# Kernel optimization log

Hardware: AMD Instinct MI355X
Metric: run time of the kernel (lower is better)

The kernel has to match this reference:

```python
import jax, jax.numpy as jnp
import numpy as np


def _conv1x1(x, W, b):
    # 1x1 conv == per-pixel channel matmul: x [B,C,H,W], W [O,C], b [O]
    return jnp.einsum('bchw,oc->bohw', x, W) + b[None, :, None, None]


def setup_inputs() -> dict:
    key = jax.random.key(0)
    ks = jax.random.split(key, 9)
    B, C, H, W = 16, 512, 32, 32
    s = 1.0 / np.sqrt(C)
    inp = {
        'x': jax.random.normal(ks[0], (B, C, H, W), dtype=jnp.float32),
        'Wq': jax.random.normal(ks[1], (C, C), dtype=jnp.float32) * s,
        'bq': jax.random.normal(ks[2], (C,), dtype=jnp.float32) * 0.01,
        'Wk': jax.random.normal(ks[3], (C, C), dtype=jnp.float32) * s,
        'bk': jax.random.normal(ks[4], (C,), dtype=jnp.float32) * 0.01,
        'Wv': jax.random.normal(ks[5], (C, C), dtype=jnp.float32) * s,
        'bv': jax.random.normal(ks[6], (C,), dtype=jnp.float32) * 0.01,
        'Wo': jax.random.normal(ks[7], (C, C), dtype=jnp.float32) * s,
        'bo': jax.random.normal(ks[8], (C,), dtype=jnp.float32) * 0.01,
    }
    return inp


def reference(x, Wq, bq, Wk, bk, Wv, bv, Wo, bo):
    B, C, H, W = x.shape
    q = _conv1x1(x, Wq, bq)
    k = _conv1x1(x, Wk, bk)
    v = _conv1x1(x, Wv, bv)
    hw = H * W
    qf = q.reshape(B, C, hw)  # [B,C,HW]
    kf = k.reshape(B, C, hw)
    vf = v.reshape(B, C, hw)
    # scores[b,i,j] = sum_c q[b,c,i] * k[b,c,j], scaled by c^-0.5
    scores = jnp.einsum('bci,bcj->bij', qf, kf) * (C ** -0.5)
    attn = jax.nn.softmax(scores, axis=2)  # softmax over keys j
    # out[b,c,i] = sum_j v[b,c,j] * attn[b,i,j]
    out = jnp.einsum('bcj,bij->bci', vf, attn).reshape(B, C, H, W)
    out = _conv1x1(out, Wo, bo)
    return x + out
```

## Files before the change

kernel.cpp:

```cpp
#include <hip/hip_runtime.h>
#include <hip/hip_bf16.h>
#include <math.h>


typedef __bf16 bf16x8 __attribute__((ext_vector_type(8)));
typedef float  f32x16 __attribute__((ext_vector_type(16)));

__device__ __forceinline__ unsigned short f2bf(float f) {
    unsigned u = __float_as_uint(f);
    u += 0x7fff + ((u >> 16) & 1);
    return (unsigned short)(u >> 16);
}

__device__ __forceinline__ void gload_lds16(const void* g, void* l) {
    __builtin_amdgcn_global_load_lds(
        (const __attribute__((address_space(1))) void*)g,
        (__attribute__((address_space(3))) void*)l, 16, 0, 0);
}

struct GemmP {
    const unsigned short* A;
    const unsigned short* B;
    void* C;
    const float* bias;
    const float* resid;
    int M, N, K, ldA, ldB;
    long sA, sB, sC, sR;
    int ln_nn, ln_pb;
    float scale;
};

template<bool OUT_F32, int BIAS_MODE, bool RESID, int EXPM>
__device__ __forceinline__ void gemm_body(const GemmP p, int L,
                                          unsigned short* Als,
                                          unsigned short* Bls)
{
    const int xcd = L & 7;
    const int idx = L >> 3;
    const int bz  = xcd * 2 + (idx >> p.ln_pb);
    const int w   = idx & ((1 << p.ln_pb) - 1);
    const int m0  = (w >> p.ln_nn) << 7;
    const int n0  = (w & ((1 << p.ln_nn) - 1)) << 8;

    const unsigned short* A = p.A + bz * p.sA;
    const unsigned short* B = p.B + bz * p.sB;

    const int tid  = threadIdx.x;
    const int lane = tid & 63;
    const int wave = tid >> 6;

    const int ar = lane >> 2;
    const int ak = (((lane & 3) ^ ((ar >> 1) & 3))) * 8;

    const unsigned short* agp = A + (long)(m0 + wave * 16 + ar) * p.ldA + ak;
    const unsigned short* bgp = B + (long)(n0 + wave * 16 + ar) * p.ldB + ak;
    const long aj = 64L * p.ldA;
    const long bj = 64L * p.ldB;

    const int ln31 = lane & 31;
    const int hi   = lane >> 5;
    const int swz  = ((ln31 >> 1) & 3) << 3;
    const int koff0 = (hi * 8) ^ swz;
    const int koff1 = (16 + hi * 8) ^ swz;

    f32x16 acc[4][2] = {};
    f32x16 acc1[4] = {};
    bf16x8 ones;
    if constexpr (EXPM == 2) {
        #pragma unroll
        for (int i = 0; i < 8; ++i) ones[i] = (__bf16)1.0f;
    }

    const int nsteps = p.K >> 5;

    auto STAGE = [&](int sel) {
        unsigned short* a0 = Als + sel * 4096;
        unsigned short* b0 = Bls + sel * 8192;
        gload_lds16(agp,          a0 + wave * 512);
        gload_lds16(agp + aj,     a0 + (wave + 4) * 512);
        gload_lds16(bgp,          b0 + wave * 512);
        gload_lds16(bgp + bj,     b0 + (wave + 4) * 512);
        gload_lds16(bgp + 2 * bj, b0 + (wave + 8) * 512);
        gload_lds16(bgp + 3 * bj, b0 + (wave + 12) * 512);
        agp += 32; bgp += 32;
    };

    auto COMPUTE = [&](int sel) {
        const unsigned short* Ap = Als + sel * 4096;
        const unsigned short* Bp = Bls + sel * 8192;
        #pragma unroll
        for (int ks = 0; ks < 2; ++ks) {
            const int ko = ks ? koff1 : koff0;
            bf16x8 af[4], bfr[2];
            #pragma unroll
            for (int mt = 0; mt < 4; ++mt)
                af[mt] = *(const bf16x8*)&Ap[(mt * 32 + ln31) * 32 + ko];
            #pragma unroll
            for (int nt = 0; nt < 2; ++nt)
                bfr[nt] = *(const bf16x8*)&Bp[(wave * 64 + nt * 32 + ln31) * 32 + ko];
            if constexpr (EXPM == 2) {
                #pragma unroll
                for (int mt = 0; mt < 4; ++mt)
                    acc1[mt] = __builtin_amdgcn_mfma_f32_32x32x16_bf16(
                        af[mt], ones, acc1[mt], 0, 0, 0);
            }
            #pragma unroll
            for (int mt = 0; mt < 4; ++mt)
                #pragma unroll
                for (int nt = 0; nt < 2; ++nt)
                    acc[mt][nt] = __builtin_amdgcn_mfma_f32_32x32x16_bf16(
                        af[mt], bfr[nt], acc[mt][nt], 0, 0, 0);
        }
    };

    STAGE(0);
    STAGE(1);

    int bc = 0, bn = 1, bs = 2;
    for (int t = 0; t < nsteps - 1; ++t) {
        __builtin_amdgcn_sched_barrier(0);
        asm volatile("s_waitcnt vmcnt(6)" ::: "memory");
        __builtin_amdgcn_s_barrier();
        asm volatile("" ::: "memory");
        __builtin_amdgcn_sched_barrier(0);
        if (t + 2 < nsteps) STAGE(bs);
        COMPUTE(bc);
        const int tmp = bc; bc = bn; bn = bs; bs = tmp;
    }
    __builtin_amdgcn_sched_barrier(0);
    asm volatile("s_waitcnt vmcnt(0)" ::: "memory");
    __builtin_amdgcn_s_barrier();
    asm volatile("" ::: "memory");
    __builtin_amdgcn_sched_barrier(0);
    COMPUTE(bc);

    float* Cf = (float*)p.C + bz * p.sC;
    unsigned short* Ch = (unsigned short*)p.C + bz * p.sC;
    const float* resid = RESID ? (p.resid + bz * p.sR) : nullptr;
    const int N = p.N;

    #pragma unroll
    for (int mt = 0; mt < 4; ++mt) {
        #pragma unroll
        for (int r = 0; r < 16; ++r) {
            const int row = m0 + mt * 32 + (r & 3) + 8 * (r >> 2) + 4 * hi;
            float rv = 0.0f;
            if constexpr (EXPM == 2) rv = 1.0f / acc1[mt][r];
            const float bm = (BIAS_MODE == 1) ? p.bias[row] : 0.0f;
            #pragma unroll
            for (int nt = 0; nt < 2; ++nt) {
                const int col = n0 + wave * 64 + nt * 32 + ln31;
                float val = acc[mt][nt][r];
                if constexpr (EXPM == 1) {
                    val = __expf(val * p.scale);
                } else {
                    if (BIAS_MODE == 1) val += bm;
                    if (BIAS_MODE == 2) val += p.bias[col];
                    if constexpr (EXPM == 2) val *= rv;
                }
                const long o = (long)row * N + col;
                if (RESID) val += resid[o];
                if (OUT_F32) Cf[o] = val;
                else         Ch[o] = f2bf(val);
            }
        }
    }
}

template<bool OUT_F32, int BIAS_MODE, bool RESID, int EXPM>
__global__ __launch_bounds__(256, 2) void gemm_bt_mfma(GemmP p)
{
    __shared__ unsigned short Als[3 * 4096];
    __shared__ unsigned short Bls[3 * 8192];
    gemm_body<OUT_F32, BIAS_MODE, RESID, EXPM>(p, blockIdx.x, Als, Bls);
}

__global__ __launch_bounds__(256, 2) void gemm_qkv_fused(GemmP pqk, GemmP pv, int split)
{
    __shared__ unsigned short Als[3 * 4096];
    __shared__ unsigned short Bls[3 * 8192];
    if ((int)blockIdx.x < split)
        gemm_body<false, 2, false, 0>(pqk, blockIdx.x, Als, Bls);
    else
        gemm_body<false, 1, false, 0>(pv, blockIdx.x - split, Als, Bls);
}

__global__ __launch_bounds__(256) void prep_all(
    const float* __restrict__ x, unsigned short* __restrict__ xT,
    const float* __restrict__ Wq, const float* __restrict__ Wk,
    const float* __restrict__ Wv, const float* __restrict__ Wo,
    const float* __restrict__ bq, const float* __restrict__ bk,
    unsigned short* __restrict__ Wb, float* __restrict__ biasqk)
{
    const int b = blockIdx.x;
    const int t = threadIdx.x;
    if (b < 8192) {
        __shared__ float tl[32][33];
        const int batch = b >> 9;
        const int rem = b & 511;
        const int p0 = (rem & 31) * 32;
        const int c0 = (rem >> 5) * 32;
        const float* xb = x + (long)batch * 524288;
        unsigned short* xTb = xT + (long)batch * 524288;
        const int tx = t & 31;
        const int ty = t >> 5;
        #pragma unroll
        for (int i = 0; i < 4; ++i)
            tl[ty + 8 * i][tx] = xb[(long)(c0 + ty + 8 * i) * 1024 + p0 + tx];
        __syncthreads();
        #pragma unroll
        for (int i = 0; i < 4; ++i)
            xTb[(long)(p0 + ty + 8 * i) * 512 + c0 + tx] = f2bf(tl[tx][ty + 8 * i]);
    } else if (b < 9216) {
        const int wb = b - 8192;
        const float* srcs[4] = {Wq, Wk, Wv, Wo};
        const float* s = srcs[wb >> 8];
        unsigned short* d = Wb + (long)(wb >> 8) * 262144;
        const int i = ((wb & 255) * 256 + t) * 4;
        const float4 f = *(const float4*)(s + i);
        ushort4 h;
        h.x = f2bf(f.x); h.y = f2bf(f.y); h.z = f2bf(f.z); h.w = f2bf(f.w);
        *(ushort4*)(d + i) = h;
    } else {
        biasqk[t]       = bq[t];
        biasqk[256 + t] = bq[256 + t];
        biasqk[512 + t] = bk[t];
        biasqk[768 + t] = bk[256 + t];
    }
}

extern "C" void kernel_launch(void* const* d_in, const int* in_sizes, int n_in,
                              void* d_out, int out_size, void* d_ws, size_t ws_size,
                              hipStream_t stream)
{
    const float* x  = (const float*)d_in[0];
    const float* Wq = (const float*)d_in[1];
    const float* bq = (const float*)d_in[2];
    const float* Wk = (const float*)d_in[3];
    const float* bk = (const float*)d_in[4];
    const float* Wv = (const float*)d_in[5];
    const float* bv = (const float*)d_in[6];
    const float* Wo = (const float*)d_in[7];
    const float* bo = (const float*)d_in[8];
    float* out = (float*)d_out;

    const int Bn = 16, C = 512, HW = 1024;
    const long CHW = (long)C * HW;
    const long SHW = (long)HW * HW;

    unsigned short* xT   = (unsigned short*)d_ws;
    unsigned short* qkT  = xT + Bn * CHW;
    unsigned short* vB   = qkT + Bn * SHW;
    unsigned short* expS = vB + Bn * CHW;
    unsigned short* Wb   = expS + Bn * SHW;
    float* biasqk = (float*)(Wb + 4 * 262144);
    unsigned short* OT = xT;

    unsigned short* Wvb = Wb + 2 * 262144;
    unsigned short* Wob = Wb + 3 * 262144;

    const dim3 blk(256);
    const float scale = 0.044194173824159216f;

    prep_all<<<dim3(9217), blk, 0, stream>>>(x, xT, Wq, Wk, Wv, Wo, bq, bk,
                                             Wb, biasqk);

    GemmP pqk = { xT, Wb, qkT, biasqk, nullptr,
                  HW, 2 * C, C, C, C, CHW, 0, SHW, 0, 2, 5, 0.0f };
    GemmP pv  = { Wvb, xT, vB, bv, nullptr,
                  C, HW, C, C, C, 0, CHW, CHW, 0, 2, 4, 0.0f };
    gemm_qkv_fused<<<dim3(768), blk, 0, stream>>>(pqk, pv, 512);

    GemmP ps  = { qkT, qkT + C, expS, nullptr, nullptr,
                  HW, HW, C, 2 * C, 2 * C, SHW, SHW, SHW, 0, 2, 5, scale };
    gemm_bt_mfma<false, 0, false, 1><<<dim3(512), blk, 0, stream>>>(ps);

    GemmP po  = { expS, vB, OT, nullptr, nullptr,
                  HW, C, HW, HW, HW, SHW, CHW, CHW, 0, 1, 4, 0.0f };
    gemm_bt_mfma<false, 0, false, 2><<<dim3(256), blk, 0, stream>>>(po);

    GemmP pout = { Wob, OT, out, bo, x,
                   C, HW, C, C, C, 0, CHW, CHW, CHW, 2, 4, 0.0f };
    gemm_bt_mfma<true, 1, true, 0><<<dim3(256), blk, 0, stream>>>(pout);
}
```

Baseline: 249.8 us.

## Switch GEMMs to 128x128 tiles with 16x16x32 MFMA and 2x2 wave grid

Shrinks the block output tile from 128x256 to 128x128, arranges the four waves as a 2x2 grid, and moves from 32x32x16 to 16x16x32 MFMA instructions. The LDS footprint per block is halved, launch bounds go from 2 to 3 blocks per CU, and every launch uses twice as many blocks, all aimed at better occupancy and load balance across CUs. It also drops the XOR swizzle on the LDS layout, which may bring back bank conflicts, and each block now reuses its A tile across a narrower N range. The epilogue is rewritten to match the new accumulator layout.

```diff
diff --git a/kernel.cpp b/kernel.cpp
--- a/kernel.cpp
+++ b/kernel.cpp
@@ -4,7 +4,7 @@
 
 
 typedef __bf16 bf16x8 __attribute__((ext_vector_type(8)));
-typedef float  f32x16 __attribute__((ext_vector_type(16)));
+typedef float  f32x4  __attribute__((ext_vector_type(4)));
 
 __device__ __forceinline__ unsigned short f2bf(float f) {
     unsigned u = __float_as_uint(f);
@@ -40,7 +40,7 @@
     const int bz  = xcd * 2 + (idx >> p.ln_pb);
     const int w   = idx & ((1 << p.ln_pb) - 1);
     const int m0  = (w >> p.ln_nn) << 7;
-    const int n0  = (w & ((1 << p.ln_nn) - 1)) << 8;
+    const int n0  = (w & ((1 << p.ln_nn) - 1)) << 7;
 
     const unsigned short* A = p.A + bz * p.sA;
     const unsigned short* B = p.B + bz * p.sB;
@@ -48,23 +48,22 @@
     const int tid  = threadIdx.x;
     const int lane = tid & 63;
     const int wave = tid >> 6;
+    const int wm   = wave >> 1;
+    const int wn   = wave & 1;
 
     const int ar = lane >> 2;
-    const int ak = (((lane & 3) ^ ((ar >> 1) & 3))) * 8;
+    const int ak = (lane & 3) * 8;
 
     const unsigned short* agp = A + (long)(m0 + wave * 16 + ar) * p.ldA + ak;
     const unsigned short* bgp = B + (long)(n0 + wave * 16 + ar) * p.ldB + ak;
     const long aj = 64L * p.ldA;
     const long bj = 64L * p.ldB;
 
-    const int ln31 = lane & 31;
-    const int hi   = lane >> 5;
-    const int swz  = ((ln31 >> 1) & 3) << 3;
-    const int koff0 = (hi * 8) ^ swz;
-    const int koff1 = (16 + hi * 8) ^ swz;
-
-    f32x16 acc[4][2] = {};
-    f32x16 acc1[4] = {};
+    const int fr = lane & 15;
+    const int fq = lane >> 4;
+
+    f32x4 acc[4][4] = {};
+    f32x4 acc1[4] = {};
     bf16x8 ones;
     if constexpr (EXPM == 2) {
         #pragma unroll
@@ -75,42 +74,36 @@
 
     auto STAGE = [&](int sel) {
         unsigned short* a0 = Als + sel * 4096;
-        unsigned short* b0 = Bls + sel * 8192;
-        gload_lds16(agp,          a0 + wave * 512);
-        gload_lds16(agp + aj,     a0 + (wave + 4) * 512);
-        gload_lds16(bgp,          b0 + wave * 512);
-        gload_lds16(bgp + bj,     b0 + (wave + 4) * 512);
-        gload_lds16(bgp + 2 * bj, b0 + (wave + 8) * 512);
-        gload_lds16(bgp + 3 * bj, b0 + (wave + 12) * 512);
+        unsigned short* b0 = Bls + sel * 4096;
+        gload_lds16(agp,      a0 + wave * 512);
+        gload_lds16(agp + aj, a0 + (wave + 4) * 512);
+        gload_lds16(bgp,      b0 + wave * 512);
+        gload_lds16(bgp + bj, b0 + (wave + 4) * 512);
         agp += 32; bgp += 32;
     };
 
     auto COMPUTE = [&](int sel) {
         const unsigned short* Ap = Als + sel * 4096;
-        const unsigned short* Bp = Bls + sel * 8192;
-        #pragma unroll
-        for (int ks = 0; ks < 2; ++ks) {
-            const int ko = ks ? koff1 : koff0;
-            bf16x8 af[4], bfr[2];
+        const unsigned short* Bp = Bls + sel * 4096;
+        bf16x8 af[4], bfr[4];
+        #pragma unroll
+        for (int mt = 0; mt < 4; ++mt)
+            af[mt] = *(const bf16x8*)&Ap[(wm * 64 + mt * 16 + fr) * 32 + fq * 8];
+        #pragma unroll
+        for (int nt = 0; nt < 4; ++nt)
+            bfr[nt] = *(const bf16x8*)&Bp[(wn * 64 + nt * 16 + fr) * 32 + fq * 8];
+        if constexpr (EXPM == 2) {
             #pragma unroll
             for (int mt = 0; mt < 4; ++mt)
-                af[mt] = *(const bf16x8*)&Ap[(mt * 32 + ln31) * 32 + ko];
-            #pragma unroll
-            for (int nt = 0; nt < 2; ++nt)
-                bfr[nt] = *(const bf16x8*)&Bp[(wave * 64 + nt * 32 + ln31) * 32 + ko];
-            if constexpr (EXPM == 2) {
-                #pragma unroll
-                for (int mt = 0; mt < 4; ++mt)
-                    acc1[mt] = __builtin_amdgcn_mfma_f32_32x32x16_bf16(
-                        af[mt], ones, acc1[mt], 0, 0, 0);
-            }
-            #pragma unroll
-            for (int mt = 0; mt < 4; ++mt)
-                #pragma unroll
-                for (int nt = 0; nt < 2; ++nt)
-                    acc[mt][nt] = __builtin_amdgcn_mfma_f32_32x32x16_bf16(
-                        af[mt], bfr[nt], acc[mt][nt], 0, 0, 0);
+                acc1[mt] = __builtin_amdgcn_mfma_f32_16x16x32_bf16(
+                    af[mt], ones, acc1[mt], 0, 0, 0);
         }
+        #pragma unroll
+        for (int mt = 0; mt < 4; ++mt)
+            #pragma unroll
+            for (int nt = 0; nt < 4; ++nt)
+                acc[mt][nt] = __builtin_amdgcn_mfma_f32_16x16x32_bf16(
+                    af[mt], bfr[nt], acc[mt][nt], 0, 0, 0);
     };
 
     STAGE(0);
@@ -119,7 +112,7 @@
     int bc = 0, bn = 1, bs = 2;
     for (int t = 0; t < nsteps - 1; ++t) {
         __builtin_amdgcn_sched_barrier(0);
-        asm volatile("s_waitcnt vmcnt(6)" ::: "memory");
+        asm volatile("s_waitcnt vmcnt(4)" ::: "memory");
         __builtin_amdgcn_s_barrier();
         asm volatile("" ::: "memory");
         __builtin_amdgcn_sched_barrier(0);
@@ -139,46 +132,59 @@
     const float* resid = RESID ? (p.resid + bz * p.sR) : nullptr;
     const int N = p.N;
 
-    #pragma unroll
-    for (int mt = 0; mt < 4; ++mt) {
-        #pragma unroll
-        for (int r = 0; r < 16; ++r) {
-            const int row = m0 + mt * 32 + (r & 3) + 8 * (r >> 2) + 4 * hi;
-            float rv = 0.0f;
-            if constexpr (EXPM == 2) rv = 1.0f / acc1[mt][r];
-            const float bm = (BIAS_MODE == 1) ? p.bias[row] : 0.0f;
-            #pragma unroll
-            for (int nt = 0; nt < 2; ++nt) {
-                const int col = n0 + wave * 64 + nt * 32 + ln31;
-                float val = acc[mt][nt][r];
-                if constexpr (EXPM == 1) {
-                    val = __expf(val * p.scale);
-                } else {
-                    if (BIAS_MODE == 1) val += bm;
-                    if (BIAS_MODE == 2) val += p.bias[col];
-                    if constexpr (EXPM == 2) val *= rv;
+    if constexpr (EXPM == 1) {
+        #pragma unroll
+        for (int mt = 0; mt < 4; ++mt)
+            #pragma unroll
+            for (int r = 0; r < 4; ++r) {
+                const int row = m0 + wm * 64 + mt * 16 + fq * 4 + r;
+                #pragma unroll
+                for (int nt = 0; nt < 4; ++nt) {
+                    const int col = n0 + wn * 64 + nt * 16 + fr;
+                    Ch[(long)row * N + col] = f2bf(__expf(acc[mt][nt][r] * p.scale));
                 }
-                const long o = (long)row * N + col;
-                if (RESID) val += resid[o];
-                if (OUT_F32) Cf[o] = val;
-                else         Ch[o] = f2bf(val);
+            }
+    } else {
+        #pragma unroll
+        for (int mt = 0; mt < 4; ++mt) {
+            float linv[4];
+            if constexpr (EXPM == 2) {
+                #pragma unroll
+                for (int r = 0; r < 4; ++r)
+                    linv[r] = 1.0f / acc1[mt][r];
+            }
+            #pragma unroll
+            for (int nt = 0; nt < 4; ++nt) {
+                const int col = n0 + wn * 64 + nt * 16 + fr;
+                const float bn2 = (BIAS_MODE == 2) ? p.bias[col] : 0.0f;
+                #pragma unroll
+                for (int r = 0; r < 4; ++r) {
+                    const int row = m0 + wm * 64 + mt * 16 + fq * 4 + r;
+                    float val = acc[mt][nt][r] + bn2;
+                    if (BIAS_MODE == 1) val += p.bias[row];
+                    if constexpr (EXPM == 2) val *= linv[r];
+                    const long o = (long)row * N + col;
+                    if (RESID) val += resid[o];
+                    if (OUT_F32) Cf[o] = val;
+                    else         Ch[o] = f2bf(val);
+                }
             }
         }
     }
 }
 
 template<bool OUT_F32, int BIAS_MODE, bool RESID, int EXPM>
-__global__ __launch_bounds__(256, 2) void gemm_bt_mfma(GemmP p)
+__global__ __launch_bounds__(256, 3) void gemm_bt_mfma(GemmP p)
 {
     __shared__ unsigned short Als[3 * 4096];
-    __shared__ unsigned short Bls[3 * 8192];
+    __shared__ unsigned short Bls[3 * 4096];
     gemm_body<OUT_F32, BIAS_MODE, RESID, EXPM>(p, blockIdx.x, Als, Bls);
 }
 
-__global__ __launch_bounds__(256, 2) void gemm_qkv_fused(GemmP pqk, GemmP pv, int split)
+__global__ __launch_bounds__(256, 3) void gemm_qkv_fused(GemmP pqk, GemmP pv, int split)
 {
     __shared__ unsigned short Als[3 * 4096];
-    __shared__ unsigned short Bls[3 * 8192];
+    __shared__ unsigned short Bls[3 * 4096];
     if ((int)blockIdx.x < split)
         gemm_body<false, 2, false, 0>(pqk, blockIdx.x, Als, Bls);
     else
@@ -266,20 +272,20 @@
                                              Wb, biasqk);
 
     GemmP pqk = { xT, Wb, qkT, biasqk, nullptr,
-                  HW, 2 * C, C, C, C, CHW, 0, SHW, 0, 2, 5, 0.0f };
+                  HW, 2 * C, C, C, C, CHW, 0, SHW, 0, 3, 6, 0.0f };
     GemmP pv  = { Wvb, xT, vB, bv, nullptr,
-                  C, HW, C, C, C, 0, CHW, CHW, 0, 2, 4, 0.0f };
-    gemm_qkv_fused<<<dim3(768), blk, 0, stream>>>(pqk, pv, 512);
+                  C, HW, C, C, C, 0, CHW, CHW, 0, 3, 5, 0.0f };
+    gemm_qkv_fused<<<dim3(1536), blk, 0, stream>>>(pqk, pv, 1024);
 
     GemmP ps  = { qkT, qkT + C, expS, nullptr, nullptr,
-                  HW, HW, C, 2 * C, 2 * C, SHW, SHW, SHW, 0, 2, 5, scale };
-    gemm_bt_mfma<false, 0, false, 1><<<dim3(512), blk, 0, stream>>>(ps);
+                  HW, HW, C, 2 * C, 2 * C, SHW, SHW, SHW, 0, 3, 6, scale };
+    gemm_bt_mfma<false, 0, false, 1><<<dim3(1024), blk, 0, stream>>>(ps);
 
     GemmP po  = { expS, vB, OT, nullptr, nullptr,
-                  HW, C, HW, HW, HW, SHW, CHW, CHW, 0, 1, 4, 0.0f };
-    gemm_bt_mfma<false, 0, false, 2><<<dim3(256), blk, 0, stream>>>(po);
+                  HW, C, HW, HW, HW, SHW, CHW, CHW, 0, 2, 5, 0.0f };
+    gemm_bt_mfma<false, 0, false, 2><<<dim3(512), blk, 0, stream>>>(po);
 
     GemmP pout = { Wob, OT, out, bo, x,
-                   C, HW, C, C, C, 0, CHW, CHW, CHW, 2, 4, 0.0f };
-    gemm_bt_mfma<true, 1, true, 0><<<dim3(256), blk, 0, stream>>>(pout);
-}
+                   C, HW, C, C, C, 0, CHW, CHW, CHW, 3, 5, 0.0f };
+    gemm_bt_mfma<true, 1, true, 0><<<dim3(512), blk, 0, stream>>>(pout);
+}
```

Result: faster. 219.7 us (-12.1%).
